# Kernel optimization log

Hardware: AMD Instinct MI355X
Metric: run time of the kernel (lower is better)

## Reference

```python
import jax, jax.numpy as jnp
import numpy as np

# Inverse synchrosqueezed STFT (one-integral inverse, ssqueezepy-style):
# x[n] = Re( sum_f Tx[f, n] ) * SCALE, where SCALE = 2 / g(0) for the
# analysis window g. We assume a window normalized so g(0) = 1, hence SCALE = 2.
ISSQ_SCALE = 2.0

def issq_stft_batched(two_d):
    # two_d: [B, 2, F, T]; channel 0 = real part, channel 1 = imag part of Tx.
    # Re(sum_f (re + i*im)) = sum_f re, so only the real channel contributes.
    return ISSQ_SCALE * two_d[:, 0].sum(axis=1)  # [B, T]


def setup_inputs() -> dict:
    key = jax.random.key(0)
    ks = jax.random.split(key, 7)
    B, Z, F, T, C = 64, 256, 128, 2048, 5
    return {
        "mean": jax.random.normal(ks[0], (B, Z), dtype=jnp.float32),
        "log_var": jax.random.normal(ks[1], (B, Z), dtype=jnp.float32),
        "output_rec": jax.random.normal(ks[2], (B, 2, F, T), dtype=jnp.float32),
        "output_clas": jax.random.normal(ks[3], (B, C), dtype=jnp.float32),
        "target_rec": jax.random.normal(ks[4], (B, 2, F, T), dtype=jnp.float32),
        "target_clas": jax.random.randint(ks[5], (B,), 0, C, dtype=jnp.int64),
        "batch_size": B,
        "img_size": T,
        "weight": jax.random.uniform(ks[6], (3,), dtype=jnp.float32),
    }


def reference(mean, log_var, output_rec, output_clas, target_rec, target_clas,
              batch_size, img_size, weight):
    # Batched inverse SSQ-STFT (replaces the per-sample Python loop).
    output_sig = issq_stft_batched(output_rec)  # [B, T]
    target_sig = issq_stft_batched(target_rec)  # [B, T]

    # Cross-entropy with mean reduction (torch F.cross_entropy default).
    logp = jax.nn.log_softmax(output_clas, axis=-1)
    clas_loss = -jnp.take_along_axis(logp, target_clas[:, None], axis=-1).mean()

    # VAE losses: sum-reduced MSE + KL divergence.
    mse = jnp.sum((output_sig - target_sig) ** 2)
    kld = -0.5 * jnp.sum(1.0 + log_var - mean ** 2 - jnp.exp(log_var))

    return weight[0] * mse + weight[1] * kld + weight[2] * clas_loss
```

## Files before the change

### kernel.cpp

```cpp
#include <hip/hip_runtime.h>

#define BATCH   64
#define FDIM    128
#define TDIM    2048
#define CDIM    5
#define ZN      (64 * 256)

__global__ __launch_bounds__(256) void mse_kernel(const float* __restrict__ o,
                                                  const float* __restrict__ tg,
                                                  float* __restrict__ acc) {
    int gid = blockIdx.x * 256 + threadIdx.x;
    int b = gid >> 11;
    int t = gid & (TDIM - 1);
    const float* po = o  + (size_t)b * (2 * FDIM * TDIM) + t;
    const float* pt = tg + (size_t)b * (2 * FDIM * TDIM) + t;
    float s = 0.0f;
#pragma unroll 8
    for (int f = 0; f < FDIM; ++f) {
        s += po[(size_t)f * TDIM] - pt[(size_t)f * TDIM];
    }
    float val = s * s;

    __shared__ float red[256];
    red[threadIdx.x] = val;
    __syncthreads();
#pragma unroll
    for (int off = 128; off > 0; off >>= 1) {
        if (threadIdx.x < (unsigned)off) red[threadIdx.x] += red[threadIdx.x + off];
        __syncthreads();
    }
    if (threadIdx.x == 0) atomicAdd(acc, red[0]);
}

__global__ __launch_bounds__(1024) void tail_kernel(const float* __restrict__ mean,
                                                    const float* __restrict__ log_var,
                                                    const float* __restrict__ oclas,
                                                    const int* __restrict__ tclas,
                                                    const float* __restrict__ w,
                                                    const float* __restrict__ mse_acc,
                                                    float* __restrict__ out) {
    int tid = threadIdx.x;

    float kld = 0.0f;
    for (int i = tid; i < ZN; i += 1024) {
        float m  = mean[i];
        float lv = log_var[i];
        kld += -0.5f * (1.0f + lv - m * m - expf(lv));
    }

    float cl = 0.0f;
    if (tid < BATCH) {
        const float* row = oclas + tid * CDIM;
        float mx = row[0];
#pragma unroll
        for (int c = 1; c < CDIM; ++c) mx = fmaxf(mx, row[c]);
        float se = 0.0f;
#pragma unroll
        for (int c = 0; c < CDIM; ++c) se += expf(row[c] - mx);
        int tc = tclas[tid];
        cl = -(row[tc] - mx - logf(se));
    }

    __shared__ float rk[1024];
    __shared__ float rc[1024];
    rk[tid] = kld;
    rc[tid] = cl;
    __syncthreads();
#pragma unroll
    for (int off = 512; off > 0; off >>= 1) {
        if (tid < off) {
            rk[tid] += rk[tid + off];
            rc[tid] += rc[tid + off];
        }
        __syncthreads();
    }

    if (tid == 0) {
        float mse = 4.0f * mse_acc[0];
        float clas_loss = rc[0] / (float)BATCH;
        out[0] = w[0] * mse + w[1] * rk[0] + w[2] * clas_loss;
    }
}

extern "C" void kernel_launch(void* const* d_in, const int* in_sizes, int n_in,
                              void* d_out, int out_size, void* d_ws, size_t ws_size,
                              hipStream_t stream) {
    const float* mean     = (const float*)d_in[0];
    const float* log_var  = (const float*)d_in[1];
    const float* orec     = (const float*)d_in[2];
    const float* oclas    = (const float*)d_in[3];
    const float* trec     = (const float*)d_in[4];
    const int*   tclas    = (const int*)d_in[5];
    const float* w        = (const float*)d_in[8];
    float* out            = (float*)d_out;
    float* acc            = (float*)d_ws;

    hipMemsetAsync(acc, 0, sizeof(float), stream);

    const int nCols  = BATCH * TDIM;
    const int blocks = nCols / 256;
    mse_kernel<<<blocks, 256, 0, stream>>>(orec, trec, acc);
    tail_kernel<<<1, 1024, 0, stream>>>(mean, log_var, oclas, tclas, w, acc, out);
}
```

Measured before the change: 265.0 us.

## Split frequency reduction across threads with float4 loads and deterministic partials

Restructures the MSE pass so each 256-thread block covers one batch and a 128-column time tile. The eight thread groups each sum 16 frequency rows using float4 loads, then combine through shared memory. Per-block partials are written to workspace and reduced in the tail kernel, which removes the memset and the global atomics. The goal is fewer, wider memory requests and one fewer launch, but there are now only 1024 blocks, each thread keeps more loads in flight, and the tail kernel does an extra reduction.

```diff
diff --git a/kernel.cpp b/kernel.cpp
--- a/kernel.cpp
+++ b/kernel.cpp
@@ -5,31 +5,56 @@
 #define TDIM    2048
 #define CDIM    5
 #define ZN      (64 * 256)
+#define NBLK    1024
 
-__global__ __launch_bounds__(256) void mse_kernel(const float* __restrict__ o,
-                                                  const float* __restrict__ tg,
-                                                  float* __restrict__ acc) {
-    int gid = blockIdx.x * 256 + threadIdx.x;
-    int b = gid >> 11;
-    int t = gid & (TDIM - 1);
-    const float* po = o  + (size_t)b * (2 * FDIM * TDIM) + t;
-    const float* pt = tg + (size_t)b * (2 * FDIM * TDIM) + t;
-    float s = 0.0f;
-#pragma unroll 8
-    for (int f = 0; f < FDIM; ++f) {
-        s += po[(size_t)f * TDIM] - pt[(size_t)f * TDIM];
+__global__ __launch_bounds__(256) void mse_partials(const float* __restrict__ o,
+                                                    const float* __restrict__ tg,
+                                                    float* __restrict__ partial) {
+    const int blk  = blockIdx.x;
+    const int b    = blk >> 4;
+    const int tile = blk & 15;
+    const int tid  = threadIdx.x;
+    const int fg   = tid >> 5;
+    const int tq   = tid & 31;
+
+    const size_t base = (size_t)b * (2 * FDIM * TDIM) + (size_t)(fg * 16) * TDIM
+                      + tile * 128 + tq * 4;
+    const float* po = o  + base;
+    const float* pt = tg + base;
+
+    float4 s = make_float4(0.f, 0.f, 0.f, 0.f);
+#pragma unroll
+    for (int i = 0; i < 16; ++i) {
+        float4 a = *(const float4*)(po + (size_t)i * TDIM);
+        float4 c = *(const float4*)(pt + (size_t)i * TDIM);
+        s.x += a.x - c.x;
+        s.y += a.y - c.y;
+        s.z += a.z - c.z;
+        s.w += a.w - c.w;
     }
-    float val = s * s;
 
-    __shared__ float red[256];
-    red[threadIdx.x] = val;
+    __shared__ float4 red[256];
+    __shared__ float  red2[32];
+    red[tid] = s;
     __syncthreads();
+
+    if (tid < 32) {
+        float4 c = red[tid];
 #pragma unroll
-    for (int off = 128; off > 0; off >>= 1) {
-        if (threadIdx.x < (unsigned)off) red[threadIdx.x] += red[threadIdx.x + off];
-        __syncthreads();
+        for (int g = 1; g < 8; ++g) {
+            float4 r = red[g * 32 + tid];
+            c.x += r.x; c.y += r.y; c.z += r.z; c.w += r.w;
+        }
+        red2[tid] = c.x * c.x + c.y * c.y + c.z * c.z + c.w * c.w;
     }
-    if (threadIdx.x == 0) atomicAdd(acc, red[0]);
+    __syncthreads();
+
+    if (tid == 0) {
+        float acc = 0.f;
+#pragma unroll
+        for (int i = 0; i < 32; ++i) acc += red2[i];
+        partial[blk] = acc;
+    }
 }
 
 __global__ __launch_bounds__(1024) void tail_kernel(const float* __restrict__ mean,
@@ -37,14 +62,18 @@
                                                     const float* __restrict__ oclas,
                                                     const int* __restrict__ tclas,
                                                     const float* __restrict__ w,
-                                                    const float* __restrict__ mse_acc,
+                                                    const float* __restrict__ partial,
                                                     float* __restrict__ out) {
-    int tid = threadIdx.x;
+    const int tid = threadIdx.x;
+
+    float ms = partial[tid];
 
     float kld = 0.0f;
-    for (int i = tid; i < ZN; i += 1024) {
-        float m  = mean[i];
-        float lv = log_var[i];
+#pragma unroll
+    for (int i = 0; i < ZN / 1024; ++i) {
+        int idx = tid + i * 1024;
+        float m  = mean[idx];
+        float lv = log_var[idx];
         kld += -0.5f * (1.0f + lv - m * m - expf(lv));
     }
 
@@ -61,14 +90,17 @@
         cl = -(row[tc] - mx - logf(se));
     }
 
+    __shared__ float rm[1024];
     __shared__ float rk[1024];
     __shared__ float rc[1024];
+    rm[tid] = ms;
     rk[tid] = kld;
     rc[tid] = cl;
     __syncthreads();
 #pragma unroll
     for (int off = 512; off > 0; off >>= 1) {
         if (tid < off) {
+            rm[tid] += rm[tid + off];
             rk[tid] += rk[tid + off];
             rc[tid] += rc[tid + off];
         }
@@ -76,7 +108,7 @@
     }
 
     if (tid == 0) {
-        float mse = 4.0f * mse_acc[0];
+        float mse = 4.0f * rm[0];
         float clas_loss = rc[0] / (float)BATCH;
         out[0] = w[0] * mse + w[1] * rk[0] + w[2] * clas_loss;
     }
@@ -85,20 +117,16 @@
 extern "C" void kernel_launch(void* const* d_in, const int* in_sizes, int n_in,
                               void* d_out, int out_size, void* d_ws, size_t ws_size,
                               hipStream_t stream) {
-    const float* mean     = (const float*)d_in[0];
-    const float* log_var  = (const float*)d_in[1];
-    const float* orec     = (const float*)d_in[2];
-    const float* oclas    = (const float*)d_in[3];
-    const float* trec     = (const float*)d_in[4];
-    const int*   tclas    = (const int*)d_in[5];
-    const float* w        = (const float*)d_in[8];
-    float* out            = (float*)d_out;
-    float* acc            = (float*)d_ws;
+    const float* mean    = (const float*)d_in[0];
+    const float* log_var = (const float*)d_in[1];
+    const float* orec    = (const float*)d_in[2];
+    const float* oclas   = (const float*)d_in[3];
+    const float* trec    = (const float*)d_in[4];
+    const int*   tclas   = (const int*)d_in[5];
+    const float* w       = (const float*)d_in[8];
+    float* out           = (float*)d_out;
+    float* partial       = (float*)d_ws;
 
-    hipMemsetAsync(acc, 0, sizeof(float), stream);
-
-    const int nCols  = BATCH * TDIM;
-    const int blocks = nCols / 256;
-    mse_kernel<<<blocks, 256, 0, stream>>>(orec, trec, acc);
-    tail_kernel<<<1, 1024, 0, stream>>>(mean, log_var, oclas, tclas, w, acc, out);
+    mse_partials<<<NBLK, 256, 0, stream>>>(orec, trec, partial);
+    tail_kernel<<<1, 1024, 0, stream>>>(mean, log_var, oclas, tclas, w, partial, out);
 }
```

New measurement: 262.0 us. No clear change (-1.2%).
